# Kernel optimization log

Measured on AMD Instinct MI355X. Metric: run time of the kernel, lower is better.

Reference implementation:

```python
import math
import jax, jax.numpy as jnp
import numpy as np

SR = 44100
N_HARMONICS = 64
EPS = 1e-5
LOG10 = math.log(10.0)


def scale_function(x):
    # ddsp_pytorch util.scale_function: 2 * sigmoid(x)**log(10) + 1e-7
    return 2.0 * jax.nn.sigmoid(x) ** LOG10 + 1e-7


def setup_inputs() -> dict:
    key = jax.random.key(0)
    k1, k2, k3 = jax.random.split(key, 3)
    bs, n_samples = 32, 64000
    # f0 in [80, 480] Hz so upper harmonics cross Nyquist for some frames
    f0_hz = jax.random.uniform(k1, (bs, n_samples), dtype=jnp.float32) * 400.0 + 80.0
    harmonic_amplitudes = jax.random.normal(k2, (bs, n_samples, N_HARMONICS + 1), dtype=jnp.float32)
    phase = jax.random.uniform(k3, (bs,), dtype=jnp.float32) * 2.0 * jnp.pi
    return {"f0_hz": f0_hz, "harmonic_amplitudes": harmonic_amplitudes, "phase": phase}


def reference(f0_hz, harmonic_amplitudes, phase):
    ha = scale_function(harmonic_amplitudes)            # (bs, S, H+1)
    f0 = f0_hz[..., None]                               # (bs, S, 1)
    total_amplitude = ha[..., :1]                       # (bs, S, 1)
    ha = ha[..., 1:]                                    # (bs, S, H)
    harm = jnp.arange(1, N_HARMONICS + 1, dtype=f0.dtype)  # (H,)
    # anti-alias: zero harmonics above Nyquist
    aa = (f0 * harm < SR / 2).astype(f0.dtype)
    ha_aa = ha * aa
    ha_aa = ha_aa / (jnp.sum(ha_aa, axis=-1, keepdims=True) + EPS)
    ha_aa = ha_aa * total_amplitude
    # phase integration
    omega = jnp.cumsum(2.0 * jnp.pi * f0 / SR, axis=1)  # (bs, S, 1)
    omega = omega + phase.reshape(-1, 1, 1)
    omegas = omega * harm                               # (bs, S, H)
    signal = jnp.sum(jnp.sin(omegas) * ha_aa, axis=-1)  # (bs, S)
    return signal
```

## Files before the change

kernel.cpp:

```cpp
#include <hip/hip_runtime.h>
#include <math.h>

#define N_SAMP   64000
#define BATCH    32
#define CHUNK    256
#define NCHUNK   250
#define NH       64

__global__ __launch_bounds__(256) void chunk_sum_kernel(
        const float* __restrict__ f0, double* __restrict__ csum) {
    int bx = blockIdx.x;
    int t  = threadIdx.x;
    double v = (double)f0[(long)bx * CHUNK + t];
    for (int off = 32; off > 0; off >>= 1) v += __shfl_down(v, off, 64);
    __shared__ double ws[4];
    int lane = t & 63, w = t >> 6;
    if (lane == 0) ws[w] = v;
    __syncthreads();
    if (t == 0) csum[bx] = ws[0] + ws[1] + ws[2] + ws[3];
}

__global__ __launch_bounds__(256) void chunk_scan_kernel(double* __restrict__ csum) {
    int r = blockIdx.x;
    int t = threadIdx.x;
    double orig = (t < NCHUNK) ? csum[(long)r * NCHUNK + t] : 0.0;
    double v = orig;
    int lane = t & 63, w = t >> 6;
    for (int off = 1; off < 64; off <<= 1) {
        double n = __shfl_up(v, off, 64);
        if (lane >= off) v += n;
    }
    __shared__ double wsum[4];
    if (lane == 63) wsum[w] = v;
    __syncthreads();
    double add = 0.0;
    for (int i = 0; i < w; ++i) add += wsum[i];
    v += add;
    if (t < NCHUNK) csum[(long)r * NCHUNK + t] = v - orig;
}

__device__ __forceinline__ float scale_fn(float x) {
    float e = exp2f(-1.4426950408889634f * x);
    float l = log2f(1.0f + e);
    return 2.0f * exp2f(-2.302585092994046f * l) + 1e-7f;
}

__global__ __launch_bounds__(256) void osc_kernel(
        const float* __restrict__ f0,
        const float* __restrict__ ha,
        const float* __restrict__ phase,
        const double* __restrict__ csum,
        float* __restrict__ out) {
    int bx = blockIdx.x;
    int r  = bx / NCHUNK;
    int t  = threadIdx.x;
    int lane = t & 63, w = t >> 6;

    long sbase = (long)bx * CHUNK;
    const float* hablk = ha + sbase * 65;

    float f0v  = f0[sbase + t];
    float traw = hablk[t * 65];

    double v = (double)f0v;
    for (int off = 1; off < 64; off <<= 1) {
        double n = __shfl_up(v, off, 64);
        if (lane >= off) v += n;
    }
    __shared__ double wsum[4];
    if (lane == 63) wsum[w] = v;
    __syncthreads();
    double add = 0.0;
    for (int i = 0; i < w; ++i) add += wsum[i];
    v += add + csum[bx];
    double x = v * (1.0 / 44100.0) + (double)phase[r] * 0.15915494309189535;
    x -= floor(x);
    float nu = (float)x;

    __shared__ float amp[CHUNK * 17];
    float S1 = 0.0f, S2 = 0.0f;
    const float half_sr = 22050.0f;
    int k  = t & 15;
    int sg = t >> 4;

    for (int hc = 0; hc < 4; ++hc) {
        __syncthreads();
        int hb = 1 + hc * 16 + k;
        #pragma unroll
        for (int j = 0; j < 16; ++j) {
            int s = j * 16 + sg;
            amp[s * 17 + k] = hablk[(long)s * 65 + hb];
        }
        __syncthreads();
        #pragma unroll
        for (int k2 = 0; k2 < 16; ++k2) {
            float hf = (float)(hc * 16 + k2 + 1);
            float a  = amp[t * 17 + k2];
            float wv = scale_fn(a);
            wv = (f0v * hf < half_sr) ? wv : 0.0f;
            float t1 = nu * hf;
            float fr = t1 - floorf(t1);
            float sv = __sinf(6.283185307179586f * fr);
            S1 += wv;
            S2 = fmaf(wv, sv, S2);
        }
    }

    float total = scale_fn(traw);
    out[sbase + t] = total * S2 / (S1 + 1e-5f);
}

extern "C" void kernel_launch(void* const* d_in, const int* in_sizes, int n_in,
                              void* d_out, int out_size, void* d_ws, size_t ws_size,
                              hipStream_t stream) {
    const float* f0    = (const float*)d_in[0];
    const float* ha    = (const float*)d_in[1];
    const float* phase = (const float*)d_in[2];
    float* out = (float*)d_out;
    double* csum = (double*)d_ws;

    chunk_sum_kernel<<<BATCH * NCHUNK, 256, 0, stream>>>(f0, csum);
    chunk_scan_kernel<<<BATCH, 256, 0, stream>>>(csum);
    osc_kernel<<<BATCH * NCHUNK, 256, 0, stream>>>(f0, ha, phase, csum, out);
}
```

Before: 780.0 us.

## Stage whole amplitude block in LDS with float4 copies and halve chunk size

```diff
diff --git a/kernel.cpp b/kernel.cpp
--- a/kernel.cpp
+++ b/kernel.cpp
@@ -3,34 +3,33 @@
 
 #define N_SAMP   64000
 #define BATCH    32
-#define CHUNK    256
-#define NCHUNK   250
+#define CHUNK    128
+#define NCHUNK   500
 #define NH       64
 
-__global__ __launch_bounds__(256) void chunk_sum_kernel(
+__global__ __launch_bounds__(128) void chunk_sum_kernel(
         const float* __restrict__ f0, double* __restrict__ csum) {
     int bx = blockIdx.x;
     int t  = threadIdx.x;
     double v = (double)f0[(long)bx * CHUNK + t];
     for (int off = 32; off > 0; off >>= 1) v += __shfl_down(v, off, 64);
-    __shared__ double ws[4];
-    int lane = t & 63, w = t >> 6;
-    if (lane == 0) ws[w] = v;
+    __shared__ double ws[2];
+    if ((t & 63) == 0) ws[t >> 6] = v;
     __syncthreads();
-    if (t == 0) csum[bx] = ws[0] + ws[1] + ws[2] + ws[3];
+    if (t == 0) csum[bx] = ws[0] + ws[1];
 }
 
-__global__ __launch_bounds__(256) void chunk_scan_kernel(double* __restrict__ csum) {
+__global__ __launch_bounds__(512) void chunk_scan_kernel(double* __restrict__ csum) {
     int r = blockIdx.x;
     int t = threadIdx.x;
+    int lane = t & 63, w = t >> 6;
     double orig = (t < NCHUNK) ? csum[(long)r * NCHUNK + t] : 0.0;
     double v = orig;
-    int lane = t & 63, w = t >> 6;
     for (int off = 1; off < 64; off <<= 1) {
         double n = __shfl_up(v, off, 64);
         if (lane >= off) v += n;
     }
-    __shared__ double wsum[4];
+    __shared__ double wsum[8];
     if (lane == 63) wsum[w] = v;
     __syncthreads();
     double add = 0.0;
@@ -45,7 +44,7 @@
     return 2.0f * exp2f(-2.302585092994046f * l) + 1e-7f;
 }
 
-__global__ __launch_bounds__(256) void osc_kernel(
+__global__ __launch_bounds__(128) void osc_kernel(
         const float* __restrict__ f0,
         const float* __restrict__ ha,
         const float* __restrict__ phase,
@@ -59,55 +58,50 @@
     long sbase = (long)bx * CHUNK;
     const float* hablk = ha + sbase * 65;
 
-    float f0v  = f0[sbase + t];
-    float traw = hablk[t * 65];
+    __shared__ float amp[CHUNK * 65];
+    {
+        const float4* src = (const float4*)hablk;
+        float4* dst = (float4*)amp;
+        #pragma unroll
+        for (int i = 0; i < 16; ++i)
+            dst[i * 128 + t] = src[i * 128 + t];
+        if (t < 2080 - 16 * 128)
+            dst[16 * 128 + t] = src[16 * 128 + t];
+    }
+
+    float f0v = f0[sbase + t];
 
     double v = (double)f0v;
     for (int off = 1; off < 64; off <<= 1) {
         double n = __shfl_up(v, off, 64);
         if (lane >= off) v += n;
     }
-    __shared__ double wsum[4];
+    __shared__ double wsum[2];
     if (lane == 63) wsum[w] = v;
     __syncthreads();
-    double add = 0.0;
-    for (int i = 0; i < w; ++i) add += wsum[i];
-    v += add + csum[bx];
+    if (w == 1) v += wsum[0];
+    v += csum[bx];
     double x = v * (1.0 / 44100.0) + (double)phase[r] * 0.15915494309189535;
     x -= floor(x);
     float nu = (float)x;
 
-    __shared__ float amp[CHUNK * 17];
+    float traw = amp[t * 65];
     float S1 = 0.0f, S2 = 0.0f;
     const float half_sr = 22050.0f;
-    int k  = t & 15;
-    int sg = t >> 4;
-
-    for (int hc = 0; hc < 4; ++hc) {
-        __syncthreads();
-        int hb = 1 + hc * 16 + k;
-        #pragma unroll
-        for (int j = 0; j < 16; ++j) {
-            int s = j * 16 + sg;
-            amp[s * 17 + k] = hablk[(long)s * 65 + hb];
-        }
-        __syncthreads();
-        #pragma unroll
-        for (int k2 = 0; k2 < 16; ++k2) {
-            float hf = (float)(hc * 16 + k2 + 1);
-            float a  = amp[t * 17 + k2];
-            float wv = scale_fn(a);
-            wv = (f0v * hf < half_sr) ? wv : 0.0f;
-            float t1 = nu * hf;
-            float fr = t1 - floorf(t1);
-            float sv = __sinf(6.283185307179586f * fr);
-            S1 += wv;
-            S2 = fmaf(wv, sv, S2);
-        }
+    #pragma unroll 16
+    for (int h = 0; h < 64; ++h) {
+        float hf = (float)(h + 1);
+        float a  = amp[t * 65 + 1 + h];
+        float wv = scale_fn(a);
+        wv = (f0v * hf < half_sr) ? wv : 0.0f;
+        float t1 = nu * hf;
+        float fr = t1 - floorf(t1);
+        float sv = __sinf(6.283185307179586f * fr);
+        S1 += wv;
+        S2 = fmaf(wv, sv, S2);
     }
 
-    float total = scale_fn(traw);
-    out[sbase + t] = total * S2 / (S1 + 1e-5f);
+    out[sbase + t] = scale_fn(traw) * S2 / (S1 + 1e-5f);
 }
 
 extern "C" void kernel_launch(void* const* d_in, const int* in_sizes, int n_in,
@@ -119,7 +113,7 @@
     float* out = (float*)d_out;
     double* csum = (double*)d_ws;
 
-    chunk_sum_kernel<<<BATCH * NCHUNK, 256, 0, stream>>>(f0, csum);
-    chunk_scan_kernel<<<BATCH, 256, 0, stream>>>(csum);
-    osc_kernel<<<BATCH * NCHUNK, 256, 0, stream>>>(f0, ha, phase, csum, out);
+    chunk_sum_kernel<<<BATCH * NCHUNK, CHUNK, 0, stream>>>(f0, csum);
+    chunk_scan_kernel<<<BATCH, 512, 0, stream>>>(csum);
+    osc_kernel<<<BATCH * NCHUNK, CHUNK, 0, stream>>>(f0, ha, phase, csum, out);
 }
```

Result: faster. 719.7 us (-7.7%).
